# Optimization experiments

Hardware: AMD Instinct MI355X
Metric: run time of the kernel (lower is better)

The kernel has to match this reference:

```python
import jax, jax.numpy as jnp
import numpy as np

N, M, C = 2048, 32, 1024  # persons, max_others, dim_inner


def setup_inputs() -> dict:
    key = jax.random.key(0)
    k1, k2, k3, k4, k5, k6 = jax.random.split(key, 6)
    return {
        "person_features": jax.random.normal(k1, (N, C, 1, 1), dtype=jnp.float32),
        "other_features": jax.random.normal(k2, (N, M, C, 1, 1), dtype=jnp.float32),
        "person_boxes": jax.random.uniform(k3, (N, 4), dtype=jnp.float32),
        "other_boxes": jax.random.uniform(k4, (N, M, 4), dtype=jnp.float32),
        "is_person": jnp.ones((N, M), dtype=bool),
        "W": jax.random.normal(k5, (C, 2 * C), dtype=jnp.float32) / np.sqrt(2 * C),
        "b": jax.random.normal(k6, (C,), dtype=jnp.float32) * 0.01,
    }


def reference(person_features, other_features, person_boxes, other_boxes, is_person, W, b):
    # person_features: [n, c, 1, 1]; other_features: [n, m, c, 1, 1]
    p = person_features[:, :, 0, 0]        # [n, c]
    o = other_features[:, :, :, 0, 0]      # [n, m, c]
    # Linear on concat([p, o]) == p @ Wp^T + o @ Wo^T + b with W = [Wp | Wo]
    Wp, Wo = W[:, :p.shape[1]], W[:, p.shape[1]:]
    pk = jnp.einsum('nc,dc->nd', p, Wp)            # shared across others
    ok = jnp.einsum('nmc,dc->nmd', o, Wo)
    x = pk[:, None, :] + ok + b                    # [n, m, d]
    x = jnp.max(x, axis=1)                         # max-pool over others
    return x[:, :, None, None]                     # [n, d, 1, 1]
```

## Files before the change

kernel.cpp:

```cpp
#include <hip/hip_runtime.h>
#include <hip/hip_bf16.h>


#define NN 2048
#define MM 32
#define CC 1024

typedef __attribute__((ext_vector_type(8))) __bf16 bf16x8;
typedef __attribute__((ext_vector_type(4))) float f32x4;
typedef __attribute__((ext_vector_type(8))) unsigned short u16x8;
typedef __attribute__((ext_vector_type(4))) unsigned short u16x4;

__device__ inline unsigned short f2bf(float f) {
  union { __hip_bfloat16 h; unsigned short u; } v;
  v.h = __float2bfloat16(f);
  return v.u;
}

__device__ inline void gload_lds16(const void* g, void* l) {
  __builtin_amdgcn_global_load_lds(
      (const __attribute__((address_space(1))) void*)g,
      (__attribute__((address_space(3))) void*)l, 16, 0, 0);
}

__global__ void conv_pw(const float* __restrict__ p, const float* __restrict__ W,
                        unsigned short* __restrict__ pd,
                        unsigned short* __restrict__ wp,
                        unsigned short* __restrict__ wo) {
  const int PG = (NN * CC) / 8;
  const int WG = (CC * 2 * CC) / 8;
  int i = blockIdx.x * blockDim.x + threadIdx.x;
  int stride = gridDim.x * blockDim.x;
  for (; i < PG + WG; i += stride) {
    if (i < PG) {
      const float4* s = reinterpret_cast<const float4*>(p) + (size_t)i * 2;
      float4 a = s[0], b = s[1];
      u16x8 r;
      r[0] = f2bf(a.x); r[1] = f2bf(a.y); r[2] = f2bf(a.z); r[3] = f2bf(a.w);
      r[4] = f2bf(b.x); r[5] = f2bf(b.y); r[6] = f2bf(b.z); r[7] = f2bf(b.w);
      *reinterpret_cast<u16x8*>(pd + (size_t)i * 8) = r;
    } else {
      int f = i - PG;
      int e = f * 8;
      int d = e >> 11;
      int cc = e & 2047;
      const float4* s = reinterpret_cast<const float4*>(W) + (size_t)f * 2;
      float4 a = s[0], b = s[1];
      u16x8 r;
      r[0] = f2bf(a.x); r[1] = f2bf(a.y); r[2] = f2bf(a.z); r[3] = f2bf(a.w);
      r[4] = f2bf(b.x); r[5] = f2bf(b.y); r[6] = f2bf(b.z); r[7] = f2bf(b.w);
      unsigned short* o = (cc < CC) ? (wp + (size_t)d * CC + cc)
                                    : (wo + (size_t)d * CC + (cc - CC));
      *reinterpret_cast<u16x8*>(o) = r;
    }
  }
}

__global__ void gemm_pk(const unsigned short* __restrict__ A,
                        const unsigned short* __restrict__ B,
                        const float* __restrict__ bvec,
                        float* __restrict__ out) {
  __shared__ unsigned short As[128 * 64];
  __shared__ unsigned short Bs[128 * 64];

  int nb = gridDim.x;
  int chunk = nb >> 3;
  int obid = blockIdx.x;
  int vb = (obid & 7) * chunk + (obid >> 3);
  int bcol = vb & 7;
  int brow = vb >> 3;

  int tid = threadIdx.x;
  int l = tid & 63;
  int wid = tid >> 6;
  int wr = wid >> 1, wc = wid & 1;
  int lr = l & 15;
  int lk = (l >> 4) << 3;

  const unsigned short* gA = A + (size_t)brow * 128 * CC;
  const unsigned short* gB = B + (size_t)bcol * 128 * CC;

  f32x4 acc[4][4] = {};

  for (int kt = 0; kt < 16; ++kt) {
    int k0 = kt * 64;
#pragma unroll
    for (int j = 0; j < 4; ++j) {
      int f = (j * 256 + tid) * 8;
      int r = f >> 6;
      int c = f & 63;
      gload_lds16(gA + (size_t)r * CC + k0 + c, &As[f]);
      gload_lds16(gB + (size_t)r * CC + k0 + c, &Bs[f]);
    }
    __syncthreads();
#pragma unroll
    for (int kk = 0; kk < 2; ++kk) {
      bf16x8 af[4], bfr[4];
#pragma unroll
      for (int mi = 0; mi < 4; ++mi)
        af[mi] = *reinterpret_cast<const bf16x8*>(
            &As[(wr * 64 + mi * 16 + lr) * 64 + kk * 32 + lk]);
#pragma unroll
      for (int ni = 0; ni < 4; ++ni)
        bfr[ni] = *reinterpret_cast<const bf16x8*>(
            &Bs[(wc * 64 + ni * 16 + lr) * 64 + kk * 32 + lk]);
#pragma unroll
      for (int mi = 0; mi < 4; ++mi)
#pragma unroll
        for (int ni = 0; ni < 4; ++ni)
          acc[mi][ni] = __builtin_amdgcn_mfma_f32_16x16x32_bf16(
              af[mi], bfr[ni], acc[mi][ni], 0, 0, 0);
    }
    __syncthreads();
  }

#pragma unroll
  for (int mi = 0; mi < 4; ++mi) {
    int row = brow * 128 + wr * 64 + mi * 16 + (l >> 4) * 4;
#pragma unroll
    for (int ni = 0; ni < 4; ++ni) {
      int col = bcol * 128 + wc * 64 + ni * 16 + lr;
      float bb = bvec[col];
#pragma unroll
      for (int r = 0; r < 4; ++r)
        out[(size_t)(row + r) * CC + col] = acc[mi][ni][r] + bb;
    }
  }
}


#define BARRIER                                      \
  do {                                               \
    asm volatile("" ::: "memory");                   \
    __builtin_amdgcn_s_barrier();                    \
    asm volatile("" ::: "memory");                   \
  } while (0)

#define LGKM0 asm volatile("s_waitcnt lgkmcnt(0)" ::: "memory")
#define VMCNT(n) asm volatile("s_waitcnt vmcnt(" #n ")" ::: "memory")

#define STAGE(gsrc, bufidx, isB, h, k0)                                       \
  do {                                                                        \
    _Pragma("unroll") for (int ii = 0; ii < 2; ++ii)                          \
        gload_lds16(gsrc + (size_t)((h) * 128 + ii * 64 + rr) * CC + (k0) + sc, \
                    lds + (bufidx) * 65536 + (isB) * 32768 + (h) * 16384 +    \
                        ii * 8192 + tid * 16);                                \
  } while (0)

#define ISSUE_A(aI, k0)                                                       \
  do {                                                                        \
    _Pragma("unroll") for (int j = 0; j < 8; ++j)                             \
        aI[j] = *reinterpret_cast<const float4*>(                             \
            gAf + (size_t)(j * 32 + arow0) * CC + (k0) + ac4 * 4);            \
  } while (0)

#define CVT_WRITE_A(aC, bufidx)                                               \
  do {                                                                        \
    _Pragma("unroll") for (int j = 0; j < 8; ++j) {                           \
      u16x4 r;                                                                \
      r[0] = f2bf(aC[j].x); r[1] = f2bf(aC[j].y);                             \
      r[2] = f2bf(aC[j].z); r[3] = f2bf(aC[j].w);                             \
      *reinterpret_cast<u16x4*>(lds + (bufidx) * 65536 +                      \
                                (j * 32 + arow0) * 128 + aswz) = r;           \
    }                                                                         \
  } while (0)

#define DSREAD_A(bufo, mq, AF)                                                \
  do {                                                                        \
    _Pragma("unroll") for (int i = 0; i < 4; ++i) {                           \
      AF[i][0] = *(const bf16x8*)(lds + (bufo) + a_base0 + (mq) * 8192 + i * 2048); \
      AF[i][1] = *(const bf16x8*)(lds + (bufo) + a_base1 + (mq) * 8192 + i * 2048); \
    }                                                                         \
  } while (0)

#define DSREAD_B(bufo, nq)                                                    \
  do {                                                                        \
    _Pragma("unroll") for (int j = 0; j < 2; ++j) {                           \
      bfr[(nq) * 2 + j][0] =                                                  \
          *(const bf16x8*)(lds + (bufo) + b_base0 + ((nq) * 2 + j) * 2048);   \
      bfr[(nq) * 2 + j][1] =                                                  \
          *(const bf16x8*)(lds + (bufo) + b_base1 + ((nq) * 2 + j) * 2048);   \
    }                                                                         \
  } while (0)

#define MFMA16(AF, mq, nq)                                                    \
  do {                                                                        \
    __builtin_amdgcn_s_setprio(1);                                            \
    _Pragma("unroll") for (int i = 0; i < 4; ++i)                             \
        _Pragma("unroll") for (int j = 0; j < 2; ++j) {                       \
      acc[(mq) * 4 + i][(nq) * 2 + j] = __builtin_amdgcn_mfma_f32_16x16x32_bf16( \
          AF[i][0], bfr[(nq) * 2 + j][0], acc[(mq) * 4 + i][(nq) * 2 + j], 0, 0, 0); \
      acc[(mq) * 4 + i][(nq) * 2 + j] = __builtin_amdgcn_mfma_f32_16x16x32_bf16( \
          AF[i][1], bfr[(nq) * 2 + j][1], acc[(mq) * 4 + i][(nq) * 2 + j], 0, 0, 0); \
    }                                                                         \
    __builtin_amdgcn_s_setprio(0);                                            \
  } while (0)

#define TILE(t, bufo)                                                         \
  do {                                                                        \
    DSREAD_A(bufo, 0, af);                                                    \
    DSREAD_B(bufo, 0);                                                        \
    BARRIER; LGKM0;                                                           \
    MFMA16(af, 0, 0);                                                         \
    BARRIER;                                                                  \
    DSREAD_B(bufo, 1);                                                        \
    if ((t) + 1 < 16) {                                                       \
      VMCNT(4);                                                               \
      CVT_WRITE_A(aL, (((t) + 1) & 1));                                       \
      if ((t) + 2 < 16) ISSUE_A(aL, ((t) + 2) * 64);                          \
    }                                                                         \
    BARRIER; LGKM0;                                                           \
    MFMA16(af, 0, 1);                                                         \
    BARRIER;                                                                  \
    DSREAD_A(bufo, 1, af2);                                                   \
    if ((t) + 2 < 16) {                                                       \
      STAGE(gB, ((t) & 1), 1, 0, ((t) + 2) * 64);                             \
      STAGE(gB, ((t) & 1), 1, 1, ((t) + 2) * 64);                             \
    }                                                                         \
    BARRIER; LGKM0;                                                           \
    MFMA16(af2, 1, 0);                                                        \
    BARRIER;                                                                  \
    MFMA16(af2, 1, 1);                                                        \
    if ((t) <= 13) { VMCNT(12); }                                             \
    else if ((t) == 14) { VMCNT(0); }                                         \
    BARRIER;                                                                  \
  } while (0)

__global__ __launch_bounds__(512, 2) void gemm_fused(
    const float* __restrict__ A,
    const unsigned short* __restrict__ B,
    const float* __restrict__ pkb,
    float* __restrict__ out) {
  __shared__ char lds[131072];

  int obid = blockIdx.x;
  int vb = (obid & 7) * 128 + (obid >> 3);
  int bcol = vb & 3;
  int brow = vb >> 2;

  int tid = threadIdx.x;
  int l = tid & 63;
  int wid = tid >> 6;
  int wr = wid >> 2;
  int wc = wid & 3;
  int lr = l & 15;
  int g = l >> 4;

  const float* gAf = A + (size_t)brow * 256 * CC;
  const unsigned short* gB = B + (size_t)bcol * 256 * CC;

  int rr = tid >> 3;
  int sc = ((tid & 7) ^ (rr & 7)) * 8;

  int arow0 = tid >> 4;
  int ac4 = tid & 15;
  int aswz = (((ac4 >> 1) ^ (arow0 & 7)) * 16) + (ac4 & 1) * 8;

  int axor = lr & 7;
  int a_base0 = (wr * 128 + lr) * 128 + ((g ^ axor) * 16);
  int a_base1 = (wr * 128 + lr) * 128 + (((4 + g) ^ axor) * 16);
  int b_base0 = 32768 + (wc * 64 + lr) * 128 + ((g ^ axor) * 16);
  int b_base1 = 32768 + (wc * 64 + lr) * 128 + (((4 + g) ^ axor) * 16);

  f32x4 acc[8][4] = {};
  bf16x8 af[4][2], af2[4][2];
  bf16x8 bfr[4][2];
  float4 aL[8];

  ISSUE_A(aL, 0);
  STAGE(gB, 0, 1, 0, 0);
  STAGE(gB, 0, 1, 1, 0);
  VMCNT(4);
  CVT_WRITE_A(aL, 0);
  ISSUE_A(aL, 64);
  STAGE(gB, 1, 1, 0, 64);
  STAGE(gB, 1, 1, 1, 64);
  VMCNT(12);
  LGKM0; BARRIER;

#pragma unroll 1
  for (int tt = 0; tt < 16; tt += 2) {
    TILE(tt, 0);
    TILE(tt + 1, 65536);
  }

  int colb = bcol * 256 + wc * 64;
#pragma unroll
  for (int a = 0; a < 4; ++a) {
    int n = brow * 8 + wr * 4 + a;
#pragma unroll
    for (int ni = 0; ni < 4; ++ni) {
      float v = -3.402823466e38f;
#pragma unroll
      for (int mi = 2 * a; mi < 2 * a + 2; ++mi)
#pragma unroll
        for (int r = 0; r < 4; ++r) v = fmaxf(v, acc[mi][ni][r]);
      v = fmaxf(v, __shfl_xor(v, 16));
      v = fmaxf(v, __shfl_xor(v, 32));
      if (l < 16) {
        int col = colb + ni * 16 + l;
        out[(size_t)n * CC + col] = v + pkb[(size_t)n * CC + col];
      }
    }
  }
}

extern "C" void kernel_launch(void* const* d_in, const int* in_sizes, int n_in,
                              void* d_out, int out_size, void* d_ws, size_t ws_size,
                              hipStream_t stream) {
  const float* p = (const float*)d_in[0];
  const float* o = (const float*)d_in[1];
  const float* W = (const float*)d_in[5];
  const float* b = (const float*)d_in[6];
  float* out = (float*)d_out;

  char* ws = (char*)d_ws;
  unsigned short* p_bf  = (unsigned short*)ws;
  unsigned short* wp_bf = (unsigned short*)(ws + 4194304);
  unsigned short* wo_bf = (unsigned short*)(ws + 6291456);
  float*          pkb   = (float*)(ws + 8388608);

  conv_pw<<<512, 256, 0, stream>>>(p, W, p_bf, wp_bf, wo_bf);
  gemm_pk<<<128, 256, 0, stream>>>(p_bf, wp_bf, b, pkb);
  gemm_fused<<<1024, 512, 0, stream>>>(o, wo_bf, pkb, out);
}
```

Baseline: 203.4 us.

## Cut per-tile barriers and prefetch next tile's A fragments into registers

Reorganizes the main GEMM tile loop so both B fragment halves are read into separate register sets at the start of each tile. The next tile's first A fragments are prefetched from LDS at the end of the current tile. This cuts the barriers per tile from seven to one, aiming to remove synchronization stalls between MFMA groups and overlap LDS reads with matrix math. It raises register pressure. It also relies on waves seeing other threads' async LDS loads without an explicit barrier after the vmcnt wait, which risks a data race.

```diff
diff --git a/kernel.cpp b/kernel.cpp
--- a/kernel.cpp
+++ b/kernel.cpp
@@ -154,13 +154,13 @@
             gAf + (size_t)(j * 32 + arow0) * CC + (k0) + ac4 * 4);            \
   } while (0)
 
-#define CVT_WRITE_A(aC, bufidx)                                               \
+#define CVT_WRITE_A(aC, bofs)                                                 \
   do {                                                                        \
     _Pragma("unroll") for (int j = 0; j < 8; ++j) {                           \
       u16x4 r;                                                                \
       r[0] = f2bf(aC[j].x); r[1] = f2bf(aC[j].y);                             \
       r[2] = f2bf(aC[j].z); r[3] = f2bf(aC[j].w);                             \
-      *reinterpret_cast<u16x4*>(lds + (bufidx) * 65536 +                      \
+      *reinterpret_cast<u16x4*>(lds + (bofs) +                                \
                                 (j * 32 + arow0) * 128 + aswz) = r;           \
     }                                                                         \
   } while (0)
@@ -173,57 +173,54 @@
     }                                                                         \
   } while (0)
 
-#define DSREAD_B(bufo, nq)                                                    \
+#define DSREAD_B(bufo, nq, BF)                                                \
   do {                                                                        \
     _Pragma("unroll") for (int j = 0; j < 2; ++j) {                           \
-      bfr[(nq) * 2 + j][0] =                                                  \
-          *(const bf16x8*)(lds + (bufo) + b_base0 + ((nq) * 2 + j) * 2048);   \
-      bfr[(nq) * 2 + j][1] =                                                  \
-          *(const bf16x8*)(lds + (bufo) + b_base1 + ((nq) * 2 + j) * 2048);   \
-    }                                                                         \
-  } while (0)
-
-#define MFMA16(AF, mq, nq)                                                    \
+      BF[j][0] = *(const bf16x8*)(lds + (bufo) + b_base0 + ((nq) * 2 + j) * 2048); \
+      BF[j][1] = *(const bf16x8*)(lds + (bufo) + b_base1 + ((nq) * 2 + j) * 2048); \
+    }                                                                         \
+  } while (0)
+
+#define MFMA16(AF, mq, nq, BF)                                                \
   do {                                                                        \
     __builtin_amdgcn_s_setprio(1);                                            \
     _Pragma("unroll") for (int i = 0; i < 4; ++i)                             \
         _Pragma("unroll") for (int j = 0; j < 2; ++j) {                       \
       acc[(mq) * 4 + i][(nq) * 2 + j] = __builtin_amdgcn_mfma_f32_16x16x32_bf16( \
-          AF[i][0], bfr[(nq) * 2 + j][0], acc[(mq) * 4 + i][(nq) * 2 + j], 0, 0, 0); \
+          AF[i][0], BF[j][0], acc[(mq) * 4 + i][(nq) * 2 + j], 0, 0, 0);      \
       acc[(mq) * 4 + i][(nq) * 2 + j] = __builtin_amdgcn_mfma_f32_16x16x32_bf16( \
-          AF[i][1], bfr[(nq) * 2 + j][1], acc[(mq) * 4 + i][(nq) * 2 + j], 0, 0, 0); \
+          AF[i][1], BF[j][1], acc[(mq) * 4 + i][(nq) * 2 + j], 0, 0, 0);      \
     }                                                                         \
     __builtin_amdgcn_s_setprio(0);                                            \
   } while (0)
 
-#define TILE(t, bufo)                                                         \
-  do {                                                                        \
-    DSREAD_A(bufo, 0, af);                                                    \
-    DSREAD_B(bufo, 0);                                                        \
-    BARRIER; LGKM0;                                                           \
-    MFMA16(af, 0, 0);                                                         \
-    BARRIER;                                                                  \
-    DSREAD_B(bufo, 1);                                                        \
+#define TILE(t, bufo, bufn)                                                   \
+  do {                                                                        \
+                                                                     \
+    DSREAD_B(bufo, 0, bfr0);                                                  \
+    DSREAD_B(bufo, 1, bfr1);                                                  \
+    MFMA16(af, 0, 0, bfr0);                                                   \
+                                                                     \
     if ((t) + 1 < 16) {                                                       \
       VMCNT(4);                                                               \
-      CVT_WRITE_A(aL, (((t) + 1) & 1));                                       \
+      CVT_WRITE_A(aL, bufn);                                                  \
       if ((t) + 2 < 16) ISSUE_A(aL, ((t) + 2) * 64);                          \
     }                                                                         \
-    BARRIER; LGKM0;                                                           \
-    MFMA16(af, 0, 1);                                                         \
+    DSREAD_A(bufo, 1, af2);                                                   \
+    MFMA16(af, 0, 1, bfr1);                                                   \
+    LGKM0;                                                                    \
     BARRIER;                                                                  \
-    DSREAD_A(bufo, 1, af2);                                                   \
+                                                                     \
     if ((t) + 2 < 16) {                                                       \
       STAGE(gB, ((t) & 1), 1, 0, ((t) + 2) * 64);                             \
       STAGE(gB, ((t) & 1), 1, 1, ((t) + 2) * 64);                             \
     }                                                                         \
-    BARRIER; LGKM0;                                                           \
-    MFMA16(af2, 1, 0);                                                        \
-    BARRIER;                                                                  \
-    MFMA16(af2, 1, 1);                                                        \
+    MFMA16(af2, 1, 0, bfr0);                                                  \
+                                                                     \
     if ((t) <= 13) { VMCNT(12); }                                             \
     else if ((t) == 14) { VMCNT(0); }                                         \
-    BARRIER;                                                                  \
+    if ((t) + 1 < 16) DSREAD_A(bufn, 0, af);                                  \
+    MFMA16(af2, 1, 1, bfr1);                                                  \
   } while (0)
 
 __global__ __launch_bounds__(512, 2) void gemm_fused(
@@ -264,7 +261,7 @@
 
   f32x4 acc[8][4] = {};
   bf16x8 af[4][2], af2[4][2];
-  bf16x8 bfr[4][2];
+  bf16x8 bfr0[2][2], bfr1[2][2];
   float4 aL[8];
 
   ISSUE_A(aL, 0);
@@ -277,11 +274,12 @@
   STAGE(gB, 1, 1, 1, 64);
   VMCNT(12);
   LGKM0; BARRIER;
+  DSREAD_A(0, 0, af);
 
 #pragma unroll 1
   for (int tt = 0; tt < 16; tt += 2) {
-    TILE(tt, 0);
-    TILE(tt + 1, 65536);
+    TILE(tt, 0, 65536);
+    TILE(tt + 1, 65536, 0);
   }
 
   int colb = bcol * 256 + wc * 64;
```

Result: slower. 360.2 us (+77.1%).
